# Optimization experiments

Measured on AMD Instinct MI355X. Metric: run time of the kernel, lower is better.

The kernel has to match this reference:

```python
import jax, jax.numpy as jnp
import numpy as np

N = 100_000      # nodes
E = 1_600_000    # edges (avg degree 16)
H = 2            # heads
C = 32           # out channels per head
L = 4            # EGAT layers
IN = 4           # input one-hot dim (node labels)
ECLS = 5         # edge classes (ratings)
SCALE = 0.1


def setup_inputs() -> dict:
    key = jax.random.key(0)
    ks = jax.random.split(key, 8)
    # node labels arange%4 -> equal user (0) / item (1) counts; x is one-hot (input_embedding=False)
    labels = jnp.arange(N) % 4
    x = jax.nn.one_hot(labels, IN, dtype=jnp.float32)
    edge_index = jax.random.randint(ks[0], (2, E), 0, N)
    edge_attr = jax.random.randint(ks[1], (E,), 0, ECLS)
    W0 = jax.random.normal(ks[2], (IN, H * C), dtype=jnp.float32) * SCALE
    W13 = jax.random.normal(ks[3], (L - 1, H * C, H * C), dtype=jnp.float32) * SCALE
    eemb = jax.random.normal(ks[4], (L, ECLS, H * C), dtype=jnp.float32) * SCALE
    att_src = jax.random.normal(ks[5], (L, H, C), dtype=jnp.float32) * SCALE
    att_dst = jax.random.normal(ks[6], (L, H, C), dtype=jnp.float32) * SCALE
    bias = jnp.zeros((L, H * C), dtype=jnp.float32)
    return dict(x=x, W0=W0, W13=W13, eemb=eemb, att_src=att_src,
                att_dst=att_dst, bias=bias, edge_index=edge_index, edge_attr=edge_attr)


def _egat_layer(x, W, eemb_l, a_src, a_dst, b, src, dst, edge_attr):
    # x: [N, Fin] -> h: [N, H, C]
    h = (x @ W).reshape(N, H, C)
    e = eemb_l[edge_attr].reshape(E, H, C)            # per-edge type embedding
    m = h[src] + e                                    # [E, H, C] edge-featured message
    logits = jax.nn.leaky_relu(
        jnp.sum(h[dst] * a_dst, axis=-1) + jnp.sum(m * a_src, axis=-1), 0.2)  # [E, H]
    # ragged softmax over incoming edges of each destination node
    amax = jax.ops.segment_max(logits, dst, num_segments=N)
    amax = jnp.where(jnp.isfinite(amax), amax, 0.0)
    ex = jnp.exp(logits - amax[dst])
    denom = jax.ops.segment_sum(ex, dst, num_segments=N)
    alpha = ex / (denom[dst] + 1e-16)                 # [E, H]
    out = jax.ops.segment_sum(alpha[..., None] * m, dst, num_segments=N)  # [N, H, C]
    return jax.nn.elu(out.reshape(N, H * C) + b)      # concat heads + elu activation


def reference(x, W0, W13, eemb, att_src, att_dst, bias, edge_index, edge_attr):
    src, dst = edge_index[0], edge_index[1]
    h = _egat_layer(x, W0, eemb[0], att_src[0], att_dst[0], bias[0], src, dst, edge_attr)
    for l in range(1, L):
        h = _egat_layer(h, W13[l - 1], eemb[l], att_src[l], att_dst[l], bias[l], src, dst, edge_attr)
    # users are nodes with label 0 (x[:,0]==1), items label 1 (x[:,1]==1);
    # labels were built as arange(N)%4, so user/item indices are static strided slices.
    user_idx = jnp.arange(0, N, 4)
    item_idx = jnp.arange(1, N, 4)
    u = h[user_idx]
    v = h[item_idx]
    return jnp.sum(u * v, axis=-1)  # MF decoder, multiply_by=1
```

## Files before the change

kernel.cpp:

```cpp
#include <hip/hip_runtime.h>
#include <hip/hip_bf16.h>
#include <math.h>

#define N_NODES 100000
#define N_EDGES 1600000
#define HC 64
#define NHEADS 2
#define NLAYERS 4
#define ECLS 5
#define NBUCK 196
#define NBLK 256
#define EPB (N_EDGES / NBLK)
#define NGRP (N_NODES / 16)

typedef __attribute__((ext_vector_type(8))) short short8;
typedef __attribute__((ext_vector_type(4))) float floatx4;
union F8 { uint4 u; short8 s; };

__device__ inline float bf_lo(unsigned int u) { return __uint_as_float(u << 16); }
__device__ inline float bf_hi(unsigned int u) { return __uint_as_float(u & 0xffff0000u); }
__device__ inline unsigned short f2bf(float f) {
    unsigned int u = __float_as_uint(f);
    u += 0x7FFFu + ((u >> 16) & 1u);
    return (unsigned short)(u >> 16);
}


__global__ void k_chist(const int* __restrict__ dst, int* __restrict__ bh) {
    __shared__ int lh[NBUCK];
    int tid = threadIdx.x, blk = blockIdx.x;
    for (int i = tid; i < NBUCK; i += 256) lh[i] = 0;
    __syncthreads();
    int s = blk * EPB, e = s + EPB;
    for (int i = s + tid; i < e; i += 256) atomicAdd(&lh[dst[i] >> 9], 1);
    __syncthreads();
    for (int i = tid; i < NBUCK; i += 256) bh[i * 256 + blk] = lh[i];
}

__global__ void k_s1(const int* __restrict__ bh, int* __restrict__ bbase,
                     int* __restrict__ part) {
    __shared__ int tmp[256];
    int tid = threadIdx.x;
    int i = blockIdx.x * 256 + tid;
    int v = bh[i];
    tmp[tid] = v;
    __syncthreads();
    for (int off = 1; off < 256; off <<= 1) {
        int t = (tid >= off) ? tmp[tid - off] : 0;
        __syncthreads();
        tmp[tid] += t;
        __syncthreads();
    }
    bbase[i] = tmp[tid] - v;
    if (tid == 255) part[blockIdx.x] = tmp[255];
}

__global__ void k_s2(int* __restrict__ part,
                     const float* __restrict__ eemb, const float* __restrict__ att_src,
                     float* __restrict__ escore) {
    __shared__ int tmp[256];
    int tid = threadIdx.x;
    int v = (tid < NBUCK) ? part[tid] : 0;
    tmp[tid] = v;
    __syncthreads();
    for (int off = 1; off < 256; off <<= 1) {
        int t = (tid >= off) ? tmp[tid - off] : 0;
        __syncthreads();
        tmp[tid] += t;
        __syncthreads();
    }
    if (tid < NBUCK) part[tid] = tmp[tid] - v;
    if (tid >= 200 && tid < 200 + NLAYERS * ECLS * NHEADS) {
        int idx = tid - 200;
        int l = idx / (ECLS * NHEADS);
        int r = idx % (ECLS * NHEADS);
        int c = r >> 1;
        int h = r & 1;
        float s = 0.f;
        const float* ev = eemb + l * ECLS * HC + c * HC + h * 32;
        const float* av = att_src + l * HC + h * 32;
        for (int k = 0; k < 32; ++k) s += ev[k] * av[k];
        escore[idx] = s;
    }
}

__global__ void k_cscatter(const int* __restrict__ src, const int* __restrict__ dst,
                           const int* __restrict__ attr, const int* __restrict__ bbase,
                           const int* __restrict__ part, int* __restrict__ bkt) {
    __shared__ int cur[NBUCK];
    int tid = threadIdx.x, blk = blockIdx.x;
    for (int i = tid; i < NBUCK; i += 256) cur[i] = bbase[i * 256 + blk] + part[i];
    __syncthreads();
    int s0 = blk * EPB, e0 = s0 + EPB;
    for (int i = s0 + tid; i < e0; i += 256) {
        int d = dst[i];
        int b = d >> 9;
        int pos = atomicAdd(&cur[b], 1);
        bkt[pos] = src[i] | (attr[i] << 17) | ((d & 511) << 20);
    }
}

__global__ void k_fine(const int* __restrict__ part, const int* __restrict__ bkt,
                       int* __restrict__ packed, int* __restrict__ rowstart) {
    __shared__ int hist[512];
    __shared__ int cur[512];
    int b = blockIdx.x, tid = threadIdx.x;
    int base = part[b];
    int bend = (b + 1 < NBUCK) ? part[b + 1] : N_EDGES;
    int nb = bend - base;
    hist[tid] = 0;
    __syncthreads();
    for (int i = tid; i < nb; i += 512)
        atomicAdd(&hist[(bkt[base + i] >> 20) & 0x1FF], 1);
    __syncthreads();
    int v = hist[tid];
    for (int off = 1; off < 512; off <<= 1) {
        int t = (tid >= off) ? hist[tid - off] : 0;
        __syncthreads();
        hist[tid] += t;
        __syncthreads();
    }
    int excl = hist[tid] - v;
    int node = (b << 9) + tid;
    if (node <= N_NODES) rowstart[node] = base + excl;
    cur[tid] = excl;
    __syncthreads();
    for (int i = tid; i < nb; i += 512) {
        int p = bkt[base + i];
        int r = atomicAdd(&cur[(p >> 20) & 0x1FF], 1);
        packed[base + r] = p;
    }
}

__global__ void k_linear0(const float* __restrict__ in,
                          const float* __restrict__ W,
                          const float* __restrict__ asrc, const float* __restrict__ adst,
                          unsigned short* __restrict__ hcurb,
                          float* __restrict__ ssrc, float* __restrict__ sdst) {
    int j = threadIdx.x & 63;
    int wid = (blockIdx.x * 256 + threadIdx.x) >> 6;
    int nwaves = gridDim.x * 4;

    float w0 = W[0 * HC + j], w1 = W[1 * HC + j], w2 = W[2 * HC + j], w3 = W[3 * HC + j];
    int head = j >> 5;
    int c = j & 31;
    float as = asrc[head * 32 + c];
    float ad = adst[head * 32 + c];

    for (int n = wid; n < N_NODES; n += nwaves) {
        int nu = __builtin_amdgcn_readfirstlane(n);
        float4 r = *(const float4*)(in + (size_t)nu * 4);
        float acc = r.x * w0 + r.y * w1 + r.z * w2 + r.w * w3;
        hcurb[(size_t)nu * HC + j] = f2bf(acc);
        float ps = acc * as;
        float pd = acc * ad;
        for (int off = 16; off > 0; off >>= 1) {
            ps += __shfl_down(ps, off, 32);
            pd += __shfl_down(pd, off, 32);
        }
        if (c == 0) {
            ssrc[nu * 2 + head] = ps;
            sdst[nu * 2 + head] = pd;
        }
    }
}

__global__ void k_linmfma(const unsigned short* __restrict__ actB,
                          const float* __restrict__ Wl,
                          const float* __restrict__ asrc,
                          const float* __restrict__ adst,
                          unsigned short* __restrict__ hcurb,
                          float* __restrict__ ssrc, float* __restrict__ sdst) {
    __shared__ uint4 WB[512];
    __shared__ unsigned short Cb[4][1024];
    int tid = threadIdx.x;
    int lane = tid & 63;
    int w = tid >> 6;
    int q = lane >> 4;
    int c = lane & 15;

    for (int rid = tid; rid < 512; rid += 256) {
        int kk = rid >> 8;
        int t  = (rid >> 6) & 3;
        int ln = rid & 63;
        int qq = ln >> 4, cc = ln & 15;
        unsigned int u[4];
        #pragma unroll
        for (int jj = 0; jj < 4; ++jj) {
            float v0 = Wl[(kk * 32 + qq * 8 + jj * 2 + 0) * 64 + 16 * t + cc];
            float v1 = Wl[(kk * 32 + qq * 8 + jj * 2 + 1) * 64 + 16 * t + cc];
            u[jj] = (unsigned int)f2bf(v0) | ((unsigned int)f2bf(v1) << 16);
        }
        WB[rid] = make_uint4(u[0], u[1], u[2], u[3]);
    }
    __syncthreads();

    short8 bfr[2][4];
    #pragma unroll
    for (int kk = 0; kk < 2; ++kk)
        #pragma unroll
        for (int t = 0; t < 4; ++t) {
            F8 tmp; tmp.u = WB[(kk * 4 + t) * 64 + lane];
            bfr[kk][t] = tmp.s;
        }

    float as_[4], ad_[4];
    #pragma unroll
    for (int t = 0; t < 4; ++t) {
        as_[t] = asrc[16 * t + c];
        ad_[t] = adst[16 * t + c];
    }

    int wid = (blockIdx.x * 256 + tid) >> 6;
    int nwaves = gridDim.x * 4;

    for (int g = wid; g < NGRP; g += nwaves) {
        int base = g * 16;
        F8 a0, a1;
        a0.u = *(const uint4*)(actB + (size_t)(base + c) * HC + q * 8);
        a1.u = *(const uint4*)(actB + (size_t)(base + c) * HC + 32 + q * 8);

        floatx4 acc[4];
        #pragma unroll
        for (int t = 0; t < 4; ++t) {
            acc[t] = (floatx4){0.f, 0.f, 0.f, 0.f};
            acc[t] = __builtin_amdgcn_mfma_f32_16x16x32_bf16(a0.s, bfr[0][t], acc[t], 0, 0, 0);
            acc[t] = __builtin_amdgcn_mfma_f32_16x16x32_bf16(a1.s, bfr[1][t], acc[t], 0, 0, 0);
        }

        #pragma unroll
        for (int r = 0; r < 4; ++r) {
            float h0s = acc[0][r] * as_[0] + acc[1][r] * as_[1];
            float h1s = acc[2][r] * as_[2] + acc[3][r] * as_[3];
            float h0d = acc[0][r] * ad_[0] + acc[1][r] * ad_[1];
            float h1d = acc[2][r] * ad_[2] + acc[3][r] * ad_[3];
            #pragma unroll
            for (int off = 1; off < 16; off <<= 1) {
                h0s += __shfl_xor(h0s, off, 64);
                h1s += __shfl_xor(h1s, off, 64);
                h0d += __shfl_xor(h0d, off, 64);
                h1d += __shfl_xor(h1d, off, 64);
            }
            if (c == 0) {
                int node = base + q * 4 + r;
                *(float2*)(ssrc + node * 2) = make_float2(h0s, h1s);
                *(float2*)(sdst + node * 2) = make_float2(h0d, h1d);
            }
        }

        #pragma unroll
        for (int t = 0; t < 4; ++t)
            #pragma unroll
            for (int r = 0; r < 4; ++r)
                Cb[w][(q * 4 + r) * 64 + 16 * t + c] = f2bf(acc[t][r]);
        __builtin_amdgcn_wave_barrier();
        const uint4* cf = (const uint4*)&Cb[w][0];
        uint4* gout = (uint4*)(hcurb + (size_t)base * HC);
        gout[lane] = cf[lane];
        gout[64 + lane] = cf[64 + lane];
        __builtin_amdgcn_wave_barrier();
    }
}

template <bool LAST>
__global__ void k_edge(const int* __restrict__ rowstart, const int* __restrict__ packed,
                       const float* __restrict__ ssrc, const float* __restrict__ sdst,
                       const float* __restrict__ escore_l,
                       const unsigned short* __restrict__ hcurb,
                       const float* __restrict__ eemb_l,
                       const float* __restrict__ bias_l,
                       unsigned short* __restrict__ actnext, float* __restrict__ out) {
    __shared__ float lbuf[4][64];
    __shared__ float obuf[2][64];
    int w = threadIdx.x >> 6;
    int n = blockIdx.x * 4 + w;
    int lane = threadIdx.x & 63;
    int sub = lane >> 3;
    int q   = lane & 7;
    int h   = q >> 2;

    int beg = rowstart[n];
    int end = rowstart[n + 1];
    float sd = sdst[n * 2 + h];

    float4 a0 = make_float4(0.f, 0.f, 0.f, 0.f);
    float4 a1 = make_float4(0.f, 0.f, 0.f, 0.f);
    float ssum = 0.f;
    for (int i = beg + sub; i < end; i += 8) {
        int p = packed[i];
        int s = p & 0x1FFFF;
        int a = (p >> 17) & 7;
        float lg = sd + ssrc[s * 2 + h] + escore_l[a * 2 + h];
        lg = lg >= 0.f ? lg : 0.2f * lg;
        float wt = __expf(lg);
        uint4 hv = *(const uint4*)(hcurb + (size_t)s * HC + q * 8);
        const float4* ep = (const float4*)(eemb_l + a * HC + q * 8);
        float4 e0 = ep[0], e1 = ep[1];
        a0.x += wt * (bf_lo(hv.x) + e0.x);
        a0.y += wt * (bf_hi(hv.x) + e0.y);
        a0.z += wt * (bf_lo(hv.y) + e0.z);
        a0.w += wt * (bf_hi(hv.y) + e0.w);
        a1.x += wt * (bf_lo(hv.z) + e1.x);
        a1.y += wt * (bf_hi(hv.z) + e1.y);
        a1.z += wt * (bf_lo(hv.w) + e1.z);
        a1.w += wt * (bf_hi(hv.w) + e1.w);
        ssum += wt;
    }
    for (int off = 8; off < 64; off <<= 1) {
        a0.x += __shfl_xor(a0.x, off, 64);
        a0.y += __shfl_xor(a0.y, off, 64);
        a0.z += __shfl_xor(a0.z, off, 64);
        a0.w += __shfl_xor(a0.w, off, 64);
        a1.x += __shfl_xor(a1.x, off, 64);
        a1.y += __shfl_xor(a1.y, off, 64);
        a1.z += __shfl_xor(a1.z, off, 64);
        a1.w += __shfl_xor(a1.w, off, 64);
        ssum  += __shfl_xor(ssum,  off, 64);
    }
    if (sub == 0) {
        ((float4*)&lbuf[w][q * 8])[0] = a0;
        ((float4*)&lbuf[w][q * 8])[1] = a1;
    }
    float ssum_h = __shfl(ssum, (lane >> 5) * 4, 64);
    float inv = 1.f / (ssum_h + 1e-16f);
    __builtin_amdgcn_wave_barrier();
    float v = lbuf[w][lane] * inv + bias_l[lane];
    float o = v > 0.f ? v : (__expf(v) - 1.f);
    if (!LAST) {
        actnext[(size_t)n * HC + lane] = f2bf(o);
    } else {
        if (w < 2) obuf[w][lane] = o;
        __syncthreads();
        if (w == 0) {
            float p = obuf[0][lane] * obuf[1][lane];
            for (int off = 32; off > 0; off >>= 1) p += __shfl_down(p, off, 64);
            if (lane == 0) out[blockIdx.x] = p;
        }
    }
}

extern "C" void kernel_launch(void* const* d_in, const int* in_sizes, int n_in,
                              void* d_out, int out_size, void* d_ws, size_t ws_size,
                              hipStream_t stream) {
    const float* x       = (const float*)d_in[0];
    const float* W0      = (const float*)d_in[1];
    const float* W13     = (const float*)d_in[2];
    const float* eemb    = (const float*)d_in[3];
    const float* att_src = (const float*)d_in[4];
    const float* att_dst = (const float*)d_in[5];
    const float* bias    = (const float*)d_in[6];
    const int*   eidx    = (const int*)d_in[7];
    const int*   eattr   = (const int*)d_in[8];
    float* out = (float*)d_out;

    const int* src = eidx;
    const int* dst = eidx + N_EDGES;

    char* wsb = (char*)d_ws;
    size_t off = 0;
    auto alloc = [&](size_t bytes) { char* p = wsb + off; off += (bytes + 255) & ~(size_t)255; return p; };
    unsigned short* hcurb  = (unsigned short*)alloc((size_t)N_NODES * HC * 2);
    unsigned short* actB   = (unsigned short*)alloc((size_t)N_NODES * HC * 2);
    float*          ssrc   = (float*)alloc((size_t)N_NODES * 2 * 4);
    float*          sdst   = (float*)alloc((size_t)N_NODES * 2 * 4);
    float*          escore = (float*)alloc(NLAYERS * ECLS * NHEADS * 4);
    int*            bh     = (int*)alloc((size_t)NBUCK * 256 * 4);
    int*            bbase  = (int*)alloc((size_t)NBUCK * 256 * 4);
    int*            part   = (int*)alloc(256 * 4);
    int*            rowstart = (int*)alloc(((size_t)N_NODES + 1) * 4);
    int*            bkt    = (int*)alloc((size_t)N_EDGES * 4);
    int*            packed = (int*)alloc((size_t)N_EDGES * 4);

    k_chist<<<NBLK, 256, 0, stream>>>(dst, bh);
    k_s1<<<NBUCK, 256, 0, stream>>>(bh, bbase, part);
    k_s2<<<1, 256, 0, stream>>>(part, eemb, att_src, escore);
    k_cscatter<<<NBLK, 256, 0, stream>>>(src, dst, eattr, bbase, part, bkt);
    k_fine<<<NBUCK, 512, 0, stream>>>(part, bkt, packed, rowstart);

    k_linear0<<<1024, 256, 0, stream>>>(x, W0, att_src, att_dst, hcurb, ssrc, sdst);

    for (int l = 0; l < NLAYERS; ++l) {
        if (l > 0) {
            k_linmfma<<<512, 256, 0, stream>>>(
                actB, W13 + (size_t)(l - 1) * HC * HC,
                att_src + l * HC, att_dst + l * HC, hcurb, ssrc, sdst);
        }
        const float* esl = escore + l * ECLS * NHEADS;
        const float* el  = eemb + (size_t)l * ECLS * HC;
        const float* bl  = bias + l * HC;
        if (l < NLAYERS - 1)
            k_edge<false><<<N_NODES / 4, 256, 0, stream>>>(
                rowstart, packed, ssrc, sdst, esl, hcurb, el, bl, actB, nullptr);
        else
            k_edge<true><<<N_NODES / 4, 256, 0, stream>>>(
                rowstart, packed, ssrc, sdst, esl, hcurb, el, bl, nullptr, out);
    }
}
```

Baseline: 382.4 us.

## Merge layer-0 linear into histogram launch and unroll edge gather loop by two

```diff
diff --git a/kernel.cpp b/kernel.cpp
--- a/kernel.cpp
+++ b/kernel.cpp
@@ -12,6 +12,7 @@
 #define NBLK 256
 #define EPB (N_EDGES / NBLK)
 #define NGRP (N_NODES / 16)
+#define LIN0_BLOCKS 1024
 
 typedef __attribute__((ext_vector_type(8))) short short8;
 typedef __attribute__((ext_vector_type(4))) float floatx4;
@@ -25,16 +26,50 @@
     return (unsigned short)(u >> 16);
 }
 
-
-__global__ void k_chist(const int* __restrict__ dst, int* __restrict__ bh) {
-    __shared__ int lh[NBUCK];
-    int tid = threadIdx.x, blk = blockIdx.x;
-    for (int i = tid; i < NBUCK; i += 256) lh[i] = 0;
-    __syncthreads();
-    int s = blk * EPB, e = s + EPB;
-    for (int i = s + tid; i < e; i += 256) atomicAdd(&lh[dst[i] >> 9], 1);
-    __syncthreads();
-    for (int i = tid; i < NBUCK; i += 256) bh[i * 256 + blk] = lh[i];
+__global__ void k_chist_lin0(const int* __restrict__ dst, int* __restrict__ bh,
+                             const float* __restrict__ in,
+                             const float* __restrict__ W,
+                             const float* __restrict__ asrc, const float* __restrict__ adst,
+                             unsigned short* __restrict__ hcurb,
+                             float* __restrict__ ssrc, float* __restrict__ sdst) {
+    int tid = threadIdx.x;
+    if (blockIdx.x < NBLK) {
+        __shared__ int lh[NBUCK];
+        int blk = blockIdx.x;
+        for (int i = tid; i < NBUCK; i += 256) lh[i] = 0;
+        __syncthreads();
+        int s = blk * EPB, e = s + EPB;
+        for (int i = s + tid; i < e; i += 256) atomicAdd(&lh[dst[i] >> 9], 1);
+        __syncthreads();
+        for (int i = tid; i < NBUCK; i += 256) bh[i * 256 + blk] = lh[i];
+        return;
+    }
+    int j = tid & 63;
+    int wid = ((blockIdx.x - NBLK) * 256 + tid) >> 6;
+    int nwaves = LIN0_BLOCKS * 4;
+
+    float w0 = W[0 * HC + j], w1 = W[1 * HC + j], w2 = W[2 * HC + j], w3 = W[3 * HC + j];
+    int head = j >> 5;
+    int c = j & 31;
+    float as = asrc[head * 32 + c];
+    float ad = adst[head * 32 + c];
+
+    for (int n = wid; n < N_NODES; n += nwaves) {
+        int nu = __builtin_amdgcn_readfirstlane(n);
+        float4 r = *(const float4*)(in + (size_t)nu * 4);
+        float acc = r.x * w0 + r.y * w1 + r.z * w2 + r.w * w3;
+        hcurb[(size_t)nu * HC + j] = f2bf(acc);
+        float ps = acc * as;
+        float pd = acc * ad;
+        for (int off = 16; off > 0; off >>= 1) {
+            ps += __shfl_down(ps, off, 32);
+            pd += __shfl_down(pd, off, 32);
+        }
+        if (c == 0) {
+            ssrc[nu * 2 + head] = ps;
+            sdst[nu * 2 + head] = pd;
+        }
+    }
 }
 
 __global__ void k_s1(const int* __restrict__ bh, int* __restrict__ bbase,
@@ -129,39 +164,6 @@
         int p = bkt[base + i];
         int r = atomicAdd(&cur[(p >> 20) & 0x1FF], 1);
         packed[base + r] = p;
-    }
-}
-
-__global__ void k_linear0(const float* __restrict__ in,
-                          const float* __restrict__ W,
-                          const float* __restrict__ asrc, const float* __restrict__ adst,
-                          unsigned short* __restrict__ hcurb,
-                          float* __restrict__ ssrc, float* __restrict__ sdst) {
-    int j = threadIdx.x & 63;
-    int wid = (blockIdx.x * 256 + threadIdx.x) >> 6;
-    int nwaves = gridDim.x * 4;
-
-    float w0 = W[0 * HC + j], w1 = W[1 * HC + j], w2 = W[2 * HC + j], w3 = W[3 * HC + j];
-    int head = j >> 5;
-    int c = j & 31;
-    float as = asrc[head * 32 + c];
-    float ad = adst[head * 32 + c];
-
-    for (int n = wid; n < N_NODES; n += nwaves) {
-        int nu = __builtin_amdgcn_readfirstlane(n);
-        float4 r = *(const float4*)(in + (size_t)nu * 4);
-        float acc = r.x * w0 + r.y * w1 + r.z * w2 + r.w * w3;
-        hcurb[(size_t)nu * HC + j] = f2bf(acc);
-        float ps = acc * as;
-        float pd = acc * ad;
-        for (int off = 16; off > 0; off >>= 1) {
-            ps += __shfl_down(ps, off, 32);
-            pd += __shfl_down(pd, off, 32);
-        }
-        if (c == 0) {
-            ssrc[nu * 2 + head] = ps;
-            sdst[nu * 2 + head] = pd;
-        }
     }
 }
 
@@ -286,7 +288,37 @@
     float4 a0 = make_float4(0.f, 0.f, 0.f, 0.f);
     float4 a1 = make_float4(0.f, 0.f, 0.f, 0.f);
     float ssum = 0.f;
-    for (int i = beg + sub; i < end; i += 8) {
+    int i = beg + sub;
+    for (; i + 8 < end; i += 16) {
+        int p1 = packed[i];
+        int p2 = packed[i + 8];
+        int s1 = p1 & 0x1FFFF, e1a = (p1 >> 17) & 7;
+        int s2 = p2 & 0x1FFFF, e2a = (p2 >> 17) & 7;
+        uint4 hv1 = *(const uint4*)(hcurb + (size_t)s1 * HC + q * 8);
+        uint4 hv2 = *(const uint4*)(hcurb + (size_t)s2 * HC + q * 8);
+        float ss1 = ssrc[s1 * 2 + h];
+        float ss2 = ssrc[s2 * 2 + h];
+        float lg1 = sd + ss1 + escore_l[e1a * 2 + h];
+        float lg2 = sd + ss2 + escore_l[e2a * 2 + h];
+        lg1 = lg1 >= 0.f ? lg1 : 0.2f * lg1;
+        lg2 = lg2 >= 0.f ? lg2 : 0.2f * lg2;
+        float w1 = __expf(lg1);
+        float w2 = __expf(lg2);
+        const float4* ep1 = (const float4*)(eemb_l + e1a * HC + q * 8);
+        const float4* ep2 = (const float4*)(eemb_l + e2a * HC + q * 8);
+        float4 e10 = ep1[0], e11 = ep1[1];
+        float4 e20 = ep2[0], e21 = ep2[1];
+        a0.x += w1 * (bf_lo(hv1.x) + e10.x) + w2 * (bf_lo(hv2.x) + e20.x);
+        a0.y += w1 * (bf_hi(hv1.x) + e10.y) + w2 * (bf_hi(hv2.x) + e20.y);
+        a0.z += w1 * (bf_lo(hv1.y) + e10.z) + w2 * (bf_lo(hv2.y) + e20.z);
+        a0.w += w1 * (bf_hi(hv1.y) + e10.w) + w2 * (bf_hi(hv2.y) + e20.w);
+        a1.x += w1 * (bf_lo(hv1.z) + e11.x) + w2 * (bf_lo(hv2.z) + e21.x);
+        a1.y += w1 * (bf_hi(hv1.z) + e11.y) + w2 * (bf_hi(hv2.z) + e21.y);
+        a1.z += w1 * (bf_lo(hv1.w) + e11.z) + w2 * (bf_lo(hv2.w) + e21.z);
+        a1.w += w1 * (bf_hi(hv1.w) + e11.w) + w2 * (bf_hi(hv2.w) + e21.w);
+        ssum += w1 + w2;
+    }
+    if (i < end) {
         int p = packed[i];
         int s = p & 0x1FFFF;
         int a = (p >> 17) & 7;
@@ -371,13 +403,12 @@
     int*            bkt    = (int*)alloc((size_t)N_EDGES * 4);
     int*            packed = (int*)alloc((size_t)N_EDGES * 4);
 
-    k_chist<<<NBLK, 256, 0, stream>>>(dst, bh);
+    k_chist_lin0<<<NBLK + LIN0_BLOCKS, 256, 0, stream>>>(
+        dst, bh, x, W0, att_src, att_dst, hcurb, ssrc, sdst);
     k_s1<<<NBUCK, 256, 0, stream>>>(bh, bbase, part);
     k_s2<<<1, 256, 0, stream>>>(part, eemb, att_src, escore);
     k_cscatter<<<NBLK, 256, 0, stream>>>(src, dst, eattr, bbase, part, bkt);
     k_fine<<<NBUCK, 512, 0, stream>>>(part, bkt, packed, rowstart);
-
-    k_linear0<<<1024, 256, 0, stream>>>(x, W0, att_src, att_dst, hcurb, ssrc, sdst);
 
     for (int l = 0; l < NLAYERS; ++l) {
         if (l > 0) {
```

New measurement: 389.3 us. No clear change (+1.8%).
